# Kernel tuning notes

Hardware: AMD Instinct MI355X
Metric: run time of the kernel (lower is better)

Reference implementation:

```python
import jax, jax.numpy as jnp
import numpy as np

N_NODES = 20000
N_EDGES = 160000
IN_SIZE = 128
HIDDEN = 256
N_HID_LAYERS = 2
OUT_SIZE = 32
N_GRAPHS = 16
NUM_MP = 4  # BASELINE_MESSAGE_PASSING (weights SHARED across rounds: [Sequential(...)]*N)
NEG_SLOPE = 0.01  # torch.nn.LeakyReLU default
W_SCALE = 0.05


def leaky(x):
    return jnp.where(x >= 0, x, NEG_SLOPE * x)


def wide_mlp(h, Win, bin_, Wh, bh, Wout, bout):
    # Linear(in,H) + act, then N_HID_LAYERS x (Linear(H,H) + act), then Linear(H,out)
    h = leaky(h @ Win + bin_)
    for l in range(Wh.shape[0]):  # small fixed layer count
        h = leaky(h @ Wh[l] + bh[l])
    return h @ Wout + bout


def setup_inputs() -> dict:
    key = jax.random.key(0)
    ks = jax.random.split(key, 16)
    d = {
        "x": jax.random.normal(ks[0], (N_NODES, IN_SIZE), jnp.float32),
        "edge_index": jax.random.randint(ks[1], (2, N_EDGES), 0, N_NODES, jnp.int64),
        "batch": jnp.sort(jax.random.randint(ks[2], (N_NODES,), 0, N_GRAPHS, jnp.int64)),
        "enc_Win": W_SCALE * jax.random.normal(ks[3], (IN_SIZE, HIDDEN), jnp.float32),
        "enc_bin": jnp.zeros((HIDDEN,), jnp.float32),
        "enc_Wh": W_SCALE * jax.random.normal(ks[4], (N_HID_LAYERS, HIDDEN, HIDDEN), jnp.float32),
        "enc_bh": jnp.zeros((N_HID_LAYERS, HIDDEN), jnp.float32),
        "enc_Wout": W_SCALE * jax.random.normal(ks[5], (HIDDEN, HIDDEN), jnp.float32),
        "enc_bout": jnp.zeros((HIDDEN,), jnp.float32),
        "edge_W": W_SCALE * jax.random.normal(ks[6], (3 * HIDDEN, HIDDEN), jnp.float32),
        "edge_b": jnp.zeros((HIDDEN,), jnp.float32),
        "proc_Win": W_SCALE * jax.random.normal(ks[7], (HIDDEN, HIDDEN), jnp.float32),
        "proc_bin": jnp.zeros((HIDDEN,), jnp.float32),
        "proc_Wh": W_SCALE * jax.random.normal(ks[8], (N_HID_LAYERS, HIDDEN, HIDDEN), jnp.float32),
        "proc_bh": jnp.zeros((N_HID_LAYERS, HIDDEN), jnp.float32),
        "proc_Wout": W_SCALE * jax.random.normal(ks[9], (HIDDEN, HIDDEN), jnp.float32),
        "proc_bout": jnp.zeros((HIDDEN,), jnp.float32),
        "dec_Win": W_SCALE * jax.random.normal(ks[10], (3 * HIDDEN, HIDDEN), jnp.float32),
        "dec_bin": jnp.zeros((HIDDEN,), jnp.float32),
        "dec_Wh": W_SCALE * jax.random.normal(ks[11], (N_HID_LAYERS, HIDDEN, HIDDEN), jnp.float32),
        "dec_bh": jnp.zeros((N_HID_LAYERS, HIDDEN), jnp.float32),
        "dec_Wout": W_SCALE * jax.random.normal(ks[12], (HIDDEN, OUT_SIZE), jnp.float32),
        "dec_bout": jnp.zeros((OUT_SIZE,), jnp.float32),
    }
    return d


def reference(x, edge_index, batch,
              enc_Win, enc_bin, enc_Wh, enc_bh, enc_Wout, enc_bout,
              edge_W, edge_b,
              proc_Win, proc_bin, proc_Wh, proc_bh, proc_Wout, proc_bout,
              dec_Win, dec_bin, dec_Wh, dec_bh, dec_Wout, dec_bout):
    n = x.shape[0]
    # encode
    h = wide_mlp(x, enc_Win, enc_bin, enc_Wh, enc_bh, enc_Wout, enc_bout)
    # add_self_loops
    loops = jnp.arange(n, dtype=edge_index.dtype)
    ei = jnp.concatenate([edge_index, jnp.stack([loops, loops])], axis=1)
    src, dst = ei[0], ei[1]  # PyG: j = ei[0] (source), i = ei[1] (target/aggregation index)
    e = jnp.zeros((ei.shape[1], HIDDEN), h.dtype)  # edge_attr None branch -> zeros
    # BASELINE_MESSAGE_PASSING rounds, shared weights
    for _ in range(NUM_MP):
        m = jnp.concatenate([h[dst], h[src], e], axis=-1) @ edge_W + edge_b  # [E+N, H]
        h = jax.ops.segment_sum(m, dst, num_segments=n)  # aggr='add'
        h = wide_mlp(h, proc_Win, proc_bin, proc_Wh, proc_bh, proc_Wout, proc_bout)
    # global mean / max / add pooling over graphs
    sums = jax.ops.segment_sum(h, batch, num_segments=N_GRAPHS)
    cnt = jax.ops.segment_sum(jnp.ones((n, 1), h.dtype), batch, num_segments=N_GRAPHS)
    mean = sums / jnp.maximum(cnt, 1.0)
    mx = jax.ops.segment_max(h, batch, num_segments=N_GRAPHS)
    pooled = jnp.concatenate([mean, mx, sums], axis=-1)  # [G, 3H]
    out = wide_mlp(pooled, dec_Win, dec_bin, dec_Wh, dec_bh, dec_Wout, dec_bout)
    return out
```

## Files before the change

### kernel.cpp

```cpp
#include <hip/hip_runtime.h>
#include <hip/hip_bf16.h>
#include <cstdint>

#define HID 256
#define NGRAPH 16
#define NEG_SLOPE 0.01f

typedef __bf16 bf16x8 __attribute__((ext_vector_type(8)));
typedef float f32x4 __attribute__((ext_vector_type(4)));

__device__ __forceinline__ float leaky(float x) { return x >= 0.f ? x : NEG_SLOPE * x; }

__device__ __forceinline__ ushort f2b(float f) {
  uint u = __float_as_uint(f);
  uint r = (u + 0x7fffu + ((u >> 16) & 1u)) >> 16;
  return (ushort)r;
}
__device__ __forceinline__ float b2f(ushort b) { return __uint_as_float((uint)b << 16); }

__global__ __launch_bounds__(256) void k_zero_i32(int* p, int n) {
  int i = blockIdx.x * blockDim.x + threadIdx.x;
  if (i < n) p[i] = 0;
}

__global__ __launch_bounds__(256) void k_hist(const int* __restrict__ key, int* __restrict__ cnt, int ne) {
  int e = blockIdx.x * blockDim.x + threadIdx.x;
  if (e < ne) atomicAdd(&cnt[key[e]], 1);
}

__global__ __launch_bounds__(1024) void k_scan(const int* __restrict__ cnt, int* __restrict__ rowptr,
                                               int* __restrict__ cursor, int n) {
  __shared__ int sd[1024];
  int tid = threadIdx.x;
  int CH = n / 1024 + 1;
  int base = tid * CH;
  int s = 0;
  for (int i = 0; i < CH; ++i) { int idx = base + i; if (idx < n) s += cnt[idx]; }
  sd[tid] = s;
  __syncthreads();
  for (int off = 1; off < 1024; off <<= 1) {
    int v = (tid >= off) ? sd[tid - off] : 0;
    __syncthreads();
    sd[tid] += v;
    __syncthreads();
  }
  int run = (tid == 0) ? 0 : sd[tid - 1];
  for (int i = 0; i < CH; ++i) {
    int idx = base + i;
    if (idx <= n) {
      rowptr[idx] = run;
      if (idx < n) { cursor[idx] = run; run += cnt[idx]; }
    }
  }
}

__global__ __launch_bounds__(64) void k_gbounds(const int* __restrict__ batch, int n,
                                                int* __restrict__ gstart, int* __restrict__ gcnt) {
  int t = threadIdx.x;
  if (t <= NGRAPH) {
    int lo = 0, hi = n;
    while (lo < hi) { int mid = (lo + hi) >> 1; if (batch[mid] < t) lo = mid + 1; else hi = mid; }
    gstart[t] = lo;
  }
  __syncthreads();
  if (t < NGRAPH) gcnt[t] = gstart[t + 1] - gstart[t];
}

__global__ __launch_bounds__(256) void k_scatter(const int* __restrict__ src, const int* __restrict__ dst,
                                                 int* __restrict__ cursor, int* __restrict__ col, int ne) {
  int e = blockIdx.x * blockDim.x + threadIdx.x;
  if (e < ne) {
    int d = dst[e];
    int pos = atomicAdd(&cursor[d], 1);
    col[pos] = src[e];
  }
}

__global__ __launch_bounds__(256) void k_f2b(const float* __restrict__ src, ushort* __restrict__ dst, int nElem) {
  int i = (blockIdx.x * 256 + threadIdx.x) * 4;
  if (i + 3 < nElem) {
    float4 v = *(const float4*)&src[i];
    ushort4 o;
    o.x = f2b(v.x); o.y = f2b(v.y); o.z = f2b(v.z); o.w = f2b(v.w);
    *(ushort4*)&dst[i] = o;
  } else {
    for (int j = i; j < nElem; ++j) dst[j] = f2b(src[j]);
  }
}

struct WconvArgs {
  const float* src[9];
  ushort* dst[9];
  int K[9];
};

__global__ __launch_bounds__(256) void k_wconv_all(WconvArgs args) {
  __shared__ float t[32][33];
  const int e = blockIdx.z;
  const int K = args.K[e];
  const int k0 = blockIdx.x * 32;
  if (k0 >= K) return;
  const float* src = args.src[e];
  ushort* dst = args.dst[e];
  const int n0 = blockIdx.y * 32;
  const int tx = threadIdx.x & 31;
  const int ty = threadIdx.x >> 5;
#pragma unroll
  for (int r = 0; r < 4; ++r) t[ty + 8 * r][tx] = src[(size_t)(k0 + ty + 8 * r) * 256 + n0 + tx];
  __syncthreads();
#pragma unroll
  for (int r = 0; r < 4; ++r) dst[(size_t)(n0 + ty + 8 * r) * K + k0 + tx] = f2b(t[tx][ty + 8 * r]);
}

__global__ __launch_bounds__(256) void k_aggregate(const ushort* __restrict__ h, const int* __restrict__ rowptr,
                                                   const int* __restrict__ col, ushort* __restrict__ S,
                                                   ushort* __restrict__ hd, float* __restrict__ degf, int n) {
  int node = blockIdx.x * 4 + (threadIdx.x >> 6);
  if (node >= n) return;
  int lane = threadIdx.x & 63;
  const ushort4* h4 = (const ushort4*)h;
  size_t base = (size_t)node * 64 + lane;
  ushort4 self = h4[base];
  float a0 = b2f(self.x), a1 = b2f(self.y), a2 = b2f(self.z), a3 = b2f(self.w);
  float s0 = a0, s1 = a1, s2 = a2, s3 = a3;
  int beg = rowptr[node], end = rowptr[node + 1];
  int p = beg;
  for (; p + 4 <= end; p += 4) {
    int j0 = col[p], j1 = col[p + 1], j2 = col[p + 2], j3 = col[p + 3];
    ushort4 v0 = h4[(size_t)j0 * 64 + lane];
    ushort4 v1 = h4[(size_t)j1 * 64 + lane];
    ushort4 v2 = h4[(size_t)j2 * 64 + lane];
    ushort4 v3 = h4[(size_t)j3 * 64 + lane];
    s0 += b2f(v0.x) + b2f(v1.x) + b2f(v2.x) + b2f(v3.x);
    s1 += b2f(v0.y) + b2f(v1.y) + b2f(v2.y) + b2f(v3.y);
    s2 += b2f(v0.z) + b2f(v1.z) + b2f(v2.z) + b2f(v3.z);
    s3 += b2f(v0.w) + b2f(v1.w) + b2f(v2.w) + b2f(v3.w);
  }
  for (; p < end; ++p) {
    int j = col[p];
    ushort4 v = h4[(size_t)j * 64 + lane];
    s0 += b2f(v.x); s1 += b2f(v.y); s2 += b2f(v.z); s3 += b2f(v.w);
  }
  float deg = (float)(end - beg + 1);
  ushort4 so; so.x = f2b(s0); so.y = f2b(s1); so.z = f2b(s2); so.w = f2b(s3);
  ((ushort4*)S)[base] = so;
  ushort4 ho; ho.x = f2b(deg * a0); ho.y = f2b(deg * a1); ho.z = f2b(deg * a2); ho.w = f2b(deg * a3);
  ((ushort4*)hd)[base] = ho;
  if (lane == 0) degf[node] = deg;
}

struct MLPArgs {
  const ushort* A0;
  const ushort* A1;
  const ushort* W0b;
  const ushort* W[5];
  const float* bias[5];
  const float* degf;
  ushort* out;
  int ldw0;
  int actf[5];
};

template <int NL, int K0, bool DUAL>
__global__ __launch_bounds__(512, 2) void k_mlp(MLPArgs args, int M) {
  __shared__ ushort act[128 * 264];
  __shared__ __align__(16) ushort As[2][128 * 32];
  __shared__ __align__(16) ushort Bs[2][256 * 32];
  __shared__ float degs[128];

  const int m0 = blockIdx.x * 128;
  const int tid = threadIdx.x;
  const int lane = tid & 63;
  const int wid = tid >> 6;
  const int wm = wid >> 2;
  const int wn = wid & 3;
  const int rl = lane & 15;
  const int kg = lane >> 4;

  if (DUAL) {
    if (tid < 128) {
      int rr = m0 + tid; if (rr > M - 1) rr = M - 1;
      degs[tid] = args.degf[rr];
    }
  }

  const int sl = tid & 3;
  const int s_row = tid >> 2;
  const int s_kg = sl ^ ((s_row >> 1) & 3);
  const int b2_row = (tid + 512) >> 2;
  const int b2_kg = sl ^ ((b2_row >> 1) & 3);
  int ga = m0 + s_row; if (ga > M - 1) ga = M - 1;

#define STAGE_A(buf, Ap, k0s)                                                            \
  {                                                                                      \
    const ushort* sa_ = (Ap) + (size_t)ga * K0 + (k0s) + s_kg * 8;                       \
    __builtin_amdgcn_global_load_lds(                                                    \
        (const __attribute__((address_space(1))) void*)sa_,                              \
        (__attribute__((address_space(3))) void*)&As[buf][tid * 8], 16, 0, 0);           \
  }
#define STAGE_B(buf, Wp, ldw, k0s)                                                       \
  {                                                                                      \
    const ushort* s1_ = (Wp) + (size_t)s_row * (ldw) + (k0s) + s_kg * 8;                 \
    const ushort* s2_ = (Wp) + (size_t)b2_row * (ldw) + (k0s) + b2_kg * 8;               \
    __builtin_amdgcn_global_load_lds(                                                    \
        (const __attribute__((address_space(1))) void*)s1_,                              \
        (__attribute__((address_space(3))) void*)&Bs[buf][tid * 8], 16, 0, 0);           \
    __builtin_amdgcn_global_load_lds(                                                    \
        (const __attribute__((address_space(1))) void*)s2_,                              \
        (__attribute__((address_space(3))) void*)&Bs[buf][(tid + 512) * 8], 16, 0, 0);   \
  }

  int rr_[4], sA_[4], rn_[4], sB_[4];
#pragma unroll
  for (int fm = 0; fm < 4; ++fm) {
    rr_[fm] = wm * 64 + fm * 16 + rl;
    sA_[fm] = kg ^ ((rr_[fm] >> 1) & 3);
  }
#pragma unroll
  for (int fn = 0; fn < 4; ++fn) {
    rn_[fn] = wn * 64 + fn * 16 + rl;
    sB_[fn] = kg ^ ((rn_[fn] >> 1) & 3);
  }

  f32x4 acc[4][4];

  auto epilogue = [&](int L, bool toGlobal) {
    const float* bp = args.bias[L];
    const int af_ = args.actf[L];
#pragma unroll
    for (int fn = 0; fn < 4; ++fn) {
      int c = wn * 64 + fn * 16 + rl;
      float bv = bp[c];
#pragma unroll
      for (int fm = 0; fm < 4; ++fm) {
        int lrow0 = wm * 64 + fm * 16 + kg * 4;
#pragma unroll
        for (int rg = 0; rg < 4; ++rg) {
          int lrow = lrow0 + rg;
          float rs = (DUAL && L == 0) ? degs[lrow] : 1.0f;
          float v = acc[fm][fn][rg] + rs * bv;
          if (af_) v = leaky(v);
          if (toGlobal) {
            int grow = m0 + lrow;
            if (grow < M) args.out[(size_t)grow * 256 + c] = f2b(v);
          } else {
            act[lrow * 264 + c] = f2b(v);
          }
        }
      }
    }
  };

  constexpr int KS0 = K0 >> 5;
  constexpr int NT0 = DUAL ? 2 * KS0 : KS0;
#pragma unroll
  for (int i = 0; i < 4; ++i)
#pragma unroll
    for (int j = 0; j < 4; ++j) acc[i][j] = (f32x4)(0.f);

  STAGE_A(0, args.A0, 0);
  STAGE_B(0, args.W[0], args.ldw0, 0);
  __syncthreads();

#pragma unroll
  for (int t = 0; t < NT0; ++t) {
    if (t + 1 < NT0) {
      const int tp = t + 1;
      const int pass = DUAL ? (tp >= KS0 ? 1 : 0) : 0;
      const int k0s = (tp - pass * KS0) << 5;
      const ushort* Ap = pass ? args.A1 : args.A0;
      const ushort* Wp = pass ? args.W0b : args.W[0];
      STAGE_A(tp & 1, Ap, k0s);
      STAGE_B(tp & 1, Wp, args.ldw0, k0s);
    } else {
      STAGE_B(0, args.W[1], 256, 0);
    }
    const ushort* bA = &As[t & 1][0];
    const ushort* bB = &Bs[t & 1][0];
    bf16x8 afr[4], bfr[4];
#pragma unroll
    for (int fm = 0; fm < 4; ++fm) afr[fm] = *(const bf16x8*)&bA[rr_[fm] * 32 + sA_[fm] * 8];
#pragma unroll
    for (int fn = 0; fn < 4; ++fn) bfr[fn] = *(const bf16x8*)&bB[rn_[fn] * 32 + sB_[fn] * 8];
#pragma unroll
    for (int fm = 0; fm < 4; ++fm)
#pragma unroll
      for (int fn = 0; fn < 4; ++fn)
        acc[fm][fn] = __builtin_amdgcn_mfma_f32_16x16x32_bf16(afr[fm], bfr[fn], acc[fm][fn], 0, 0, 0);
    __syncthreads();
  }
  epilogue(0, NL == 1);
  __syncthreads();

  for (int L = 1; L < NL; ++L) {
#pragma unroll
    for (int i = 0; i < 4; ++i)
#pragma unroll
      for (int j = 0; j < 4; ++j) acc[i][j] = (f32x4)(0.f);
#pragma unroll
    for (int t = 0; t < 8; ++t) {
      if (t < 7) {
        STAGE_B((t + 1) & 1, args.W[L], 256, (t + 1) * 32);
      } else if (L + 1 < NL) {
        STAGE_B(0, args.W[L + 1], 256, 0);
      }
      const ushort* bB = &Bs[t & 1][0];
      bf16x8 afr[4], bfr[4];
#pragma unroll
      for (int fm = 0; fm < 4; ++fm) afr[fm] = *(const bf16x8*)&act[rr_[fm] * 264 + t * 32 + kg * 8];
#pragma unroll
      for (int fn = 0; fn < 4; ++fn) bfr[fn] = *(const bf16x8*)&bB[rn_[fn] * 32 + sB_[fn] * 8];
#pragma unroll
      for (int fm = 0; fm < 4; ++fm)
#pragma unroll
        for (int fn = 0; fn < 4; ++fn)
          acc[fm][fn] = __builtin_amdgcn_mfma_f32_16x16x32_bf16(afr[fm], bfr[fn], acc[fm][fn], 0, 0, 0);
      __syncthreads();
    }
    if (L == NL - 1) {
      epilogue(L, true);
    } else {
      epilogue(L, false);
      __syncthreads();
    }
  }
#undef STAGE_A
#undef STAGE_B
}

__global__ __launch_bounds__(256) void k_dec_layer(
    const float* __restrict__ A, const float* __restrict__ W,
    const float* __restrict__ bias, float* __restrict__ out,
    int K, int N, int act)
{
  __shared__ float a[768];
  __shared__ float red[8][64];
  const int g = blockIdx.y;
  const int cols = (N >= 64) ? 64 : 32;
  const int segs = 256 / cols;
  const int t = threadIdx.x;
  const int col = t % cols, seg = t / cols;
  const int c = blockIdx.x * cols + col;
  for (int i = t; i < K; i += 256) a[i] = A[(size_t)g * K + i];
  __syncthreads();
  const int kper = K / segs;
  const int k0 = seg * kper;
  float p = 0.f;
#pragma unroll 8
  for (int k = k0; k < k0 + kper; ++k) p += a[k] * W[(size_t)k * N + c];
  red[seg][col] = p;
  __syncthreads();
  if (seg == 0) {
    float s = bias[c];
    for (int i = 0; i < segs; ++i) s += red[i][col];
    out[(size_t)g * N + c] = act ? leaky(s) : s;
  }
}

__global__ __launch_bounds__(256) void k_pool1(const ushort* __restrict__ h, const int* __restrict__ gstart,
                                               const int* __restrict__ gcnt, float* __restrict__ psum,
                                               float* __restrict__ pmax) {
  int g = blockIdx.x >> 4;
  int cch = blockIdx.x & 15;
  int t = threadIdx.x;
  int len = gcnt[g];
  int s0 = gstart[g];
  int chunk = (len + 15) >> 4;
  int i0 = s0 + cch * chunk;
  int i1 = min(i0 + chunk, s0 + len);
  float s = 0.f;
  float m = -3.402823466e+38f;
  for (int i = i0; i < i1; ++i) {
    float v = b2f(h[(size_t)i * HID + t]);
    s += v;
    m = fmaxf(m, v);
  }
  psum[(size_t)blockIdx.x * HID + t] = s;
  pmax[(size_t)blockIdx.x * HID + t] = m;
}

__global__ __launch_bounds__(256) void k_pool2(const float* __restrict__ psum, const float* __restrict__ pmax,
                                               const int* __restrict__ gcnt, float* __restrict__ pooled) {
  int g = blockIdx.x;
  int t = threadIdx.x;
  float s = 0.f, m = -3.402823466e+38f;
  for (int cch = 0; cch < 16; ++cch) {
    s += psum[(size_t)(g * 16 + cch) * HID + t];
    m = fmaxf(m, pmax[(size_t)(g * 16 + cch) * HID + t]);
  }
  float cf = (float)gcnt[g];
  pooled[g * 3 * HID + t] = s / fmaxf(cf, 1.f);
  pooled[g * 3 * HID + HID + t] = m;
  pooled[g * 3 * HID + 2 * HID + t] = s;
}

extern "C" void kernel_launch(void* const* d_in, const int* in_sizes, int n_in,
                              void* d_out, int out_size, void* d_ws, size_t ws_size,
                              hipStream_t stream) {
  const float* x        = (const float*)d_in[0];
  const int*   ei       = (const int*)d_in[1];
  const int*   batch    = (const int*)d_in[2];
  const float* enc_Win  = (const float*)d_in[3];
  const float* enc_bin  = (const float*)d_in[4];
  const float* enc_Wh   = (const float*)d_in[5];
  const float* enc_bh   = (const float*)d_in[6];
  const float* enc_Wout = (const float*)d_in[7];
  const float* enc_bout = (const float*)d_in[8];
  const float* edge_W   = (const float*)d_in[9];
  const float* edge_b   = (const float*)d_in[10];
  const float* proc_Win = (const float*)d_in[11];
  const float* proc_bin = (const float*)d_in[12];
  const float* proc_Wh  = (const float*)d_in[13];
  const float* proc_bh  = (const float*)d_in[14];
  const float* proc_Wout= (const float*)d_in[15];
  const float* proc_bout= (const float*)d_in[16];
  const float* dec_Win  = (const float*)d_in[17];
  const float* dec_bin  = (const float*)d_in[18];
  const float* dec_Wh   = (const float*)d_in[19];
  const float* dec_bh   = (const float*)d_in[20];
  const float* dec_Wout = (const float*)d_in[21];
  const float* dec_bout = (const float*)d_in[22];

  const int n  = in_sizes[0] / 128;
  const int ne = in_sizes[1] / 2;
  const int H = HID;

  char* p = (char*)d_ws;
  auto alloc = [&](size_t bytes) -> char* {
    char* r = p;
    p += (bytes + 255) & ~(size_t)255;
    return r;
  };
  ushort* hb1   = (ushort*)alloc((size_t)n * H * 2);
  ushort* Sb    = (ushort*)alloc((size_t)n * H * 2);
  ushort* hdb   = (ushort*)alloc((size_t)n * H * 2);
  ushort* xb    = (ushort*)alloc((size_t)n * 128 * 2);
  ushort* w_enc_in  = (ushort*)alloc((size_t)256 * 128 * 2);
  ushort* w_enc_h0  = (ushort*)alloc((size_t)256 * 256 * 2);
  ushort* w_enc_h1  = (ushort*)alloc((size_t)256 * 256 * 2);
  ushort* w_enc_out = (ushort*)alloc((size_t)256 * 256 * 2);
  ushort* w_proc_in  = (ushort*)alloc((size_t)256 * 256 * 2);
  ushort* w_proc_h0  = (ushort*)alloc((size_t)256 * 256 * 2);
  ushort* w_proc_h1  = (ushort*)alloc((size_t)256 * 256 * 2);
  ushort* w_proc_out = (ushort*)alloc((size_t)256 * 256 * 2);
  ushort* w_edge     = (ushort*)alloc((size_t)256 * 512 * 2);
  float* degf   = (float*)alloc((size_t)n * 4);
  float* pooled = (float*)alloc((size_t)NGRAPH * 3 * H * 4);
  float* psum   = (float*)alloc((size_t)256 * H * 4);
  float* pmax   = (float*)alloc((size_t)256 * H * 4);
  float* db0    = (float*)alloc((size_t)NGRAPH * H * 4);
  float* db1    = (float*)alloc((size_t)NGRAPH * H * 4);
  int* cnt    = (int*)alloc((size_t)n * 4);
  int* rowptr = (int*)alloc((size_t)(n + 1) * 4);
  int* cursor = (int*)alloc((size_t)n * 4);
  int* gstart = (int*)alloc((size_t)(NGRAPH + 1) * 4);
  int* gcnt   = (int*)alloc((size_t)NGRAPH * 4);
  int* colv   = (int*)alloc((size_t)ne * 4);

  const int* srcI = ei;
  const int* dstI = ei + ne;

  dim3 blk(256);

  WconvArgs wa;
  wa.src[0] = enc_Win;             wa.dst[0] = w_enc_in;   wa.K[0] = 128;
  wa.src[1] = enc_Wh;              wa.dst[1] = w_enc_h0;   wa.K[1] = 256;
  wa.src[2] = enc_Wh + 65536;      wa.dst[2] = w_enc_h1;   wa.K[2] = 256;
  wa.src[3] = enc_Wout;            wa.dst[3] = w_enc_out;  wa.K[3] = 256;
  wa.src[4] = proc_Win;            wa.dst[4] = w_proc_in;  wa.K[4] = 256;
  wa.src[5] = proc_Wh;             wa.dst[5] = w_proc_h0;  wa.K[5] = 256;
  wa.src[6] = proc_Wh + 65536;     wa.dst[6] = w_proc_h1;  wa.K[6] = 256;
  wa.src[7] = proc_Wout;           wa.dst[7] = w_proc_out; wa.K[7] = 256;
  wa.src[8] = edge_W;              wa.dst[8] = w_edge;     wa.K[8] = 512;
  k_wconv_all<<<dim3(16, 8, 9), blk, 0, stream>>>(wa);
  k_f2b<<<dim3((n * 128 / 4 + 255) / 256), blk, 0, stream>>>(x, xb, n * 128);

  k_zero_i32<<<dim3((n + 255) / 256), blk, 0, stream>>>(cnt, n);
  k_hist<<<dim3((ne + 255) / 256), blk, 0, stream>>>(dstI, cnt, ne);
  k_scan<<<1, 1024, 0, stream>>>(cnt, rowptr, cursor, n);
  k_gbounds<<<1, 64, 0, stream>>>(batch, n, gstart, gcnt);
  k_scatter<<<dim3((ne + 255) / 256), blk, 0, stream>>>(srcI, dstI, cursor, colv, ne);

  const int npanel = (n + 127) / 128;
  dim3 mblk(512);

  MLPArgs ea = {};
  ea.A0 = xb; ea.A1 = nullptr; ea.W0b = nullptr;
  ea.W[0] = w_enc_in; ea.W[1] = w_enc_h0; ea.W[2] = w_enc_h1; ea.W[3] = w_enc_out;
  ea.bias[0] = enc_bin; ea.bias[1] = enc_bh; ea.bias[2] = enc_bh + 256; ea.bias[3] = enc_bout;
  ea.degf = nullptr; ea.out = hb1; ea.ldw0 = 128;
  ea.actf[0] = 1; ea.actf[1] = 1; ea.actf[2] = 1; ea.actf[3] = 0;
  k_mlp<4, 128, false><<<dim3(npanel), mblk, 0, stream>>>(ea, n);

  MLPArgs pa = {};
  pa.A0 = hdb; pa.A1 = Sb; pa.W0b = w_edge + 256;
  pa.W[0] = w_edge; pa.W[1] = w_proc_in; pa.W[2] = w_proc_h0; pa.W[3] = w_proc_h1; pa.W[4] = w_proc_out;
  pa.bias[0] = edge_b; pa.bias[1] = proc_bin; pa.bias[2] = proc_bh; pa.bias[3] = proc_bh + 256; pa.bias[4] = proc_bout;
  pa.degf = degf; pa.out = hb1; pa.ldw0 = 512;
  pa.actf[0] = 0; pa.actf[1] = 1; pa.actf[2] = 1; pa.actf[3] = 1; pa.actf[4] = 0;

  for (int r = 0; r < 4; ++r) {
    k_aggregate<<<dim3((n + 3) / 4), blk, 0, stream>>>(hb1, rowptr, colv, Sb, hdb, degf, n);
    k_mlp<5, 256, true><<<dim3(npanel), mblk, 0, stream>>>(pa, n);
  }

  k_pool1<<<dim3(NGRAPH * 16), blk, 0, stream>>>(hb1, gstart, gcnt, psum, pmax);
  k_pool2<<<dim3(NGRAPH), blk, 0, stream>>>(psum, pmax, gcnt, pooled);

  k_dec_layer<<<dim3(4, NGRAPH), blk, 0, stream>>>(pooled, dec_Win, dec_bin, db0, 768, 256, 1);
  k_dec_layer<<<dim3(4, NGRAPH), blk, 0, stream>>>(db0, dec_Wh, dec_bh, db1, 256, 256, 1);
  k_dec_layer<<<dim3(4, NGRAPH), blk, 0, stream>>>(db1, dec_Wh + 65536, dec_bh + 256, db0, 256, 256, 1);
  k_dec_layer<<<dim3(1, NGRAPH), blk, 0, stream>>>(db0, dec_Wout, dec_bout, (float*)d_out, 256, 32, 0);
}
```

Measured before the change: 407.6 us.

## Shrink fused MLP tile to 64 rows with 4 waves and swizzled activation LDS

The fused per-panel MLP kernel moves from 128-row tiles with 8 waves to 64-row tiles with 4 waves, which doubles the number of blocks (about 313 instead of 157) so more CUs get work. The intermediate activation buffer becomes a K-chunked, XOR-swizzled layout matching the A-operand pattern, replacing the padded row-major layout, and the LDS footprint per block shrinks. In exchange each weight tile loaded into LDS is reused across only 64 rows, so total weight traffic from L2 per row doubles.

```diff
diff --git a/kernel.cpp b/kernel.cpp
--- a/kernel.cpp
+++ b/kernel.cpp
@@ -162,33 +162,26 @@
 };
 
 template <int NL, int K0, bool DUAL>
-__global__ __launch_bounds__(512, 2) void k_mlp(MLPArgs args, int M) {
-  __shared__ ushort act[128 * 264];
-  __shared__ __align__(16) ushort As[2][128 * 32];
+__global__ __launch_bounds__(256, 2) void k_mlp(MLPArgs args, int M) {
+  __shared__ ushort act[8 * 64 * 32];
+  __shared__ __align__(16) ushort As[2][64 * 32];
   __shared__ __align__(16) ushort Bs[2][256 * 32];
-  __shared__ float degs[128];
-
-  const int m0 = blockIdx.x * 128;
+  __shared__ float degs[64];
+
+  const int m0 = blockIdx.x * 64;
   const int tid = threadIdx.x;
   const int lane = tid & 63;
-  const int wid = tid >> 6;
-  const int wm = wid >> 2;
-  const int wn = wid & 3;
+  const int wn = tid >> 6;
   const int rl = lane & 15;
   const int kg = lane >> 4;
 
-  if (DUAL) {
-    if (tid < 128) {
-      int rr = m0 + tid; if (rr > M - 1) rr = M - 1;
-      degs[tid] = args.degf[rr];
-    }
-  }
-
-  const int sl = tid & 3;
+  if (DUAL && tid < 64) {
+    int rr = m0 + tid; if (rr > M - 1) rr = M - 1;
+    degs[tid] = args.degf[rr];
+  }
+
   const int s_row = tid >> 2;
-  const int s_kg = sl ^ ((s_row >> 1) & 3);
-  const int b2_row = (tid + 512) >> 2;
-  const int b2_kg = sl ^ ((b2_row >> 1) & 3);
+  const int s_kg = (tid & 3) ^ ((s_row >> 1) & 3);
   int ga = m0 + s_row; if (ga > M - 1) ga = M - 1;
 
 #define STAGE_A(buf, Ap, k0s)                                                            \
@@ -199,21 +192,18 @@
         (__attribute__((address_space(3))) void*)&As[buf][tid * 8], 16, 0, 0);           \
   }
 #define STAGE_B(buf, Wp, ldw, k0s)                                                       \
-  {                                                                                      \
-    const ushort* s1_ = (Wp) + (size_t)s_row * (ldw) + (k0s) + s_kg * 8;                 \
-    const ushort* s2_ = (Wp) + (size_t)b2_row * (ldw) + (k0s) + b2_kg * 8;               \
+  _Pragma("unroll")                                                                      \
+  for (int i_ = 0; i_ < 4; ++i_) {                                                       \
+    const ushort* sb_ = (Wp) + (size_t)(s_row + 64 * i_) * (ldw) + (k0s) + s_kg * 8;     \
     __builtin_amdgcn_global_load_lds(                                                    \
-        (const __attribute__((address_space(1))) void*)s1_,                              \
-        (__attribute__((address_space(3))) void*)&Bs[buf][tid * 8], 16, 0, 0);           \
-    __builtin_amdgcn_global_load_lds(                                                    \
-        (const __attribute__((address_space(1))) void*)s2_,                              \
-        (__attribute__((address_space(3))) void*)&Bs[buf][(tid + 512) * 8], 16, 0, 0);   \
+        (const __attribute__((address_space(1))) void*)sb_,                              \
+        (__attribute__((address_space(3))) void*)&Bs[buf][(tid + 256 * i_) * 8], 16, 0, 0); \
   }
 
   int rr_[4], sA_[4], rn_[4], sB_[4];
 #pragma unroll
   for (int fm = 0; fm < 4; ++fm) {
-    rr_[fm] = wm * 64 + fm * 16 + rl;
+    rr_[fm] = fm * 16 + rl;
     sA_[fm] = kg ^ ((rr_[fm] >> 1) & 3);
   }
 #pragma unroll
@@ -231,9 +221,10 @@
     for (int fn = 0; fn < 4; ++fn) {
       int c = wn * 64 + fn * 16 + rl;
       float bv = bp[c];
+      int ch = c >> 5, g = (c >> 3) & 3, e = c & 7;
 #pragma unroll
       for (int fm = 0; fm < 4; ++fm) {
-        int lrow0 = wm * 64 + fm * 16 + kg * 4;
+        int lrow0 = fm * 16 + kg * 4;
 #pragma unroll
         for (int rg = 0; rg < 4; ++rg) {
           int lrow = lrow0 + rg;
@@ -244,7 +235,8 @@
             int grow = m0 + lrow;
             if (grow < M) args.out[(size_t)grow * 256 + c] = f2b(v);
           } else {
-            act[lrow * 264 + c] = f2b(v);
+            int slot = g ^ ((lrow >> 1) & 3);
+            act[ch * 2048 + lrow * 32 + slot * 8 + e] = f2b(v);
           }
         }
       }
@@ -272,7 +264,7 @@
       const ushort* Wp = pass ? args.W0b : args.W[0];
       STAGE_A(tp & 1, Ap, k0s);
       STAGE_B(tp & 1, Wp, args.ldw0, k0s);
-    } else {
+    } else if (NL > 1) {
       STAGE_B(0, args.W[1], 256, 0);
     }
     const ushort* bA = &As[t & 1][0];
@@ -290,7 +282,7 @@
     __syncthreads();
   }
   epilogue(0, NL == 1);
-  __syncthreads();
+  if (NL > 1) __syncthreads();
 
   for (int L = 1; L < NL; ++L) {
 #pragma unroll
@@ -307,7 +299,8 @@
       const ushort* bB = &Bs[t & 1][0];
       bf16x8 afr[4], bfr[4];
 #pragma unroll
-      for (int fm = 0; fm < 4; ++fm) afr[fm] = *(const bf16x8*)&act[rr_[fm] * 264 + t * 32 + kg * 8];
+      for (int fm = 0; fm < 4; ++fm)
+        afr[fm] = *(const bf16x8*)&act[t * 2048 + rr_[fm] * 32 + sA_[fm] * 8];
 #pragma unroll
       for (int fn = 0; fn < 4; ++fn) bfr[fn] = *(const bf16x8*)&bB[rn_[fn] * 32 + sB_[fn] * 8];
 #pragma unroll
@@ -481,8 +474,7 @@
   k_gbounds<<<1, 64, 0, stream>>>(batch, n, gstart, gcnt);
   k_scatter<<<dim3((ne + 255) / 256), blk, 0, stream>>>(srcI, dstI, cursor, colv, ne);
 
-  const int npanel = (n + 127) / 128;
-  dim3 mblk(512);
+  const int npanel = (n + 63) / 64;
 
   MLPArgs ea = {};
   ea.A0 = xb; ea.A1 = nullptr; ea.W0b = nullptr;
@@ -490,7 +482,7 @@
   ea.bias[0] = enc_bin; ea.bias[1] = enc_bh; ea.bias[2] = enc_bh + 256; ea.bias[3] = enc_bout;
   ea.degf = nullptr; ea.out = hb1; ea.ldw0 = 128;
   ea.actf[0] = 1; ea.actf[1] = 1; ea.actf[2] = 1; ea.actf[3] = 0;
-  k_mlp<4, 128, false><<<dim3(npanel), mblk, 0, stream>>>(ea, n);
+  k_mlp<4, 128, false><<<dim3(npanel), blk, 0, stream>>>(ea, n);
 
   MLPArgs pa = {};
   pa.A0 = hdb; pa.A1 = Sb; pa.W0b = w_edge + 256;
@@ -501,7 +493,7 @@
 
   for (int r = 0; r < 4; ++r) {
     k_aggregate<<<dim3((n + 3) / 4), blk, 0, stream>>>(hb1, rowptr, colv, Sb, hdb, degf, n);
-    k_mlp<5, 256, true><<<dim3(npanel), mblk, 0, stream>>>(pa, n);
+    k_mlp<5, 256, true><<<dim3(npanel), blk, 0, stream>>>(pa, n);
   }
 
   k_pool1<<<dim3(NGRAPH * 16), blk, 0, stream>>>(hb1, gstart, gcnt, psum, pmax);
```

Result: slower. 416.3 us (+2.1%).
